# Performance work log

Hardware: AMD Instinct MI355X
Metric: run time of the kernel (lower is better)

## Reference

```python
import jax, jax.numpy as jnp
import numpy as np

B0, PER, T, V, E = 8, 2, 128, 50257, 4
N = B0 * PER


def setup_inputs() -> dict:
    key = jax.random.key(0)
    k1, k2, k3, k4 = jax.random.split(key, 4)
    return {
        "gen_ori_img_preds": jax.random.normal(k1, (B0, T, V), dtype=jnp.float32),
        "gen_cap_preds": jax.random.normal(k2, (N, T, V), dtype=jnp.float32),
        "masked_item_lens": jnp.full((B0,), PER, dtype=jnp.int32),
        "entities_ids": jax.random.randint(k3, (N, E), 0, V, dtype=jnp.int32),
        "prefixes_lens": jax.random.randint(k4, (N,), 1, T, dtype=jnp.int32),  # unused by forward
        "prompt_length": 20,  # unused by forward
    }


def reference(gen_ori_img_preds, gen_cap_preds, masked_item_lens, entities_ids, prefixes_lens, prompt_length):
    # gen_ori_img_preds: [B0, T, V]; gen_cap_preds: [N, T, V]; entities_ids: [N, E]
    B0_, T_, _ = gen_ori_img_preds.shape
    N_ = gen_cap_preds.shape[0]
    # repeat_interleave(arange(B0), masked_item_lens) -> map each expanded row to its source sample
    repeated = jnp.repeat(jnp.arange(B0_), masked_item_lens, total_repeat_length=N_)  # [N]
    # log_softmax gathered at entity columns: log_softmax(x)[..., e] = x[..., e] - logsumexp(x)
    lse_ori = jax.nn.logsumexp(gen_ori_img_preds, axis=-1)  # [B0, T]
    lse_gen = jax.nn.logsumexp(gen_cap_preds, axis=-1)      # [N, T]
    t_idx = jnp.arange(T_)[None, :, None]
    # gather raw logits at entity ids, broadcast over T -> [N, T, E]
    g_ori = gen_ori_img_preds[repeated[:, None, None], t_idx, entities_ids[:, None, :]] \
            - lse_ori[repeated][:, :, None]
    g_gen = jnp.take_along_axis(gen_cap_preds, entities_ids[:, None, :], axis=2) \
            - lse_gen[:, :, None]
    # mean over T per entity, difference, then mean over entities (sum / len(entity_ids_i))
    per_entity = g_ori.mean(axis=1) - g_gen.mean(axis=1)  # [N, E]
    sample_loss = per_entity.mean(axis=-1)                 # [N]
    return (-sample_loss).mean()
```

## Files before the change

### kernel.cpp

```cpp
#include <hip/hip_runtime.h>

#define B0 8
#define T  128
#define V  50257
#define E  4
#define NN 16

__global__ __launch_bounds__(256) void lse_kernel(
    const float* __restrict__ ori, const float* __restrict__ cap,
    float* __restrict__ lse) {
  const int row = blockIdx.x;
  const float* base;
  long long s;
  if (row < B0 * T) {
    base = ori;
    s = (long long)row * V;
  } else {
    base = cap;
    s = (long long)(row - B0 * T) * V;
  }
  const long long end = s + V;
  const long long s_al = (s + 3) & ~3LL;
  const int tid = threadIdx.x;

  float a0 = 0.f, a1 = 0.f, a2 = 0.f, a3 = 0.f;

  const int head = (int)(s_al - s);
  if (tid < head) a0 += __expf(base[s + tid]);

  const long long n4 = (end - s_al) >> 2;
  const float4* b4 = (const float4*)(base + s_al);
  for (long long j = tid; j < n4; j += 256) {
    const float4 v = b4[j];
    a0 += __expf(v.x);
    a1 += __expf(v.y);
    a2 += __expf(v.z);
    a3 += __expf(v.w);
  }

  const long long tstart = s_al + (n4 << 2);
  const int tail = (int)(end - tstart);
  if (tid < tail) a1 += __expf(base[tstart + tid]);

  float acc = (a0 + a1) + (a2 + a3);

  __shared__ float red[256];
  red[tid] = acc;
  __syncthreads();
  for (int w = 128; w > 0; w >>= 1) {
    if (tid < w) red[tid] += red[tid + w];
    __syncthreads();
  }
  if (tid == 0) lse[row] = __logf(red[0]);
}

__global__ __launch_bounds__(256) void finish_kernel(
    const float* __restrict__ ori, const float* __restrict__ cap,
    const int* __restrict__ mlens, const int* __restrict__ eids,
    const float* __restrict__ lse, float* __restrict__ out) {
  __shared__ int rep[NN];
  const int tid = threadIdx.x;
  if (tid == 0) {
    int idx = 0;
    for (int b = 0; b < B0 && idx < NN; ++b) {
      const int c = mlens[b];
      for (int k = 0; k < c && idx < NN; ++k) rep[idx++] = b;
    }
    const int lastv = (idx > 0) ? rep[idx - 1] : 0;
    for (; idx < NN; ++idx) rep[idx] = lastv;
  }
  __syncthreads();

  const float* lse_ori = lse;
  const float* lse_gen = lse + B0 * T;

  float sg = 0.f;
  for (int i = tid; i < NN * E * T; i += 256) {
    const int n = i / (E * T);
    const int r = i - n * (E * T);
    const int e = r / T;
    const int t = r - e * T;
    const int col = eids[n * E + e];
    sg += ori[((long long)rep[n] * T + t) * V + col]
        - cap[((long long)n * T + t) * V + col];
  }

  float sl = 0.f;
  for (int i = tid; i < NN * T; i += 256) {
    const int n = i / T;
    const int t = i - n * T;
    sl += lse_gen[n * T + t] - lse_ori[rep[n] * T + t];
  }

  __shared__ float r1[256];
  __shared__ float r2[256];
  r1[tid] = sg;
  r2[tid] = sl;
  __syncthreads();
  for (int w = 128; w > 0; w >>= 1) {
    if (tid < w) {
      r1[tid] += r1[tid + w];
      r2[tid] += r2[tid + w];
    }
    __syncthreads();
  }
  if (tid == 0) {
    out[0] = -(r1[0] / (float)(NN * E * T) + r2[0] / (float)(NN * T));
  }
}

extern "C" void kernel_launch(void* const* d_in, const int* in_sizes, int n_in,
                              void* d_out, int out_size, void* d_ws, size_t ws_size,
                              hipStream_t stream) {
  const float* ori   = (const float*)d_in[0];
  const float* cap   = (const float*)d_in[1];
  const int*   mlens = (const int*)d_in[2];
  const int*   eids  = (const int*)d_in[3];
  float* out = (float*)d_out;
  float* lse = (float*)d_ws;

  const int rows = B0 * T + NN * T;
  lse_kernel<<<rows, 256, 0, stream>>>(ori, cap, lse);
  finish_kernel<<<1, 256, 0, stream>>>(ori, cap, mlens, eids, lse, out);
}
```

Measured before the change: 695.0 us.

## Fuse LSE and final reduction into one kernel with atomic last-block finish

Merges the per-row logsumexp kernel and the single-block finish kernel into one kernel. Each row block adds its own entity-logit gathers and weighted LSE contribution to a global double accumulator, and the last block to arrive, found through an atomic counter, writes the output. This removes the serial single-block tail kernel and the LSE workspace round trip, at the cost of a memset, per-block atomics and a changed floating-point summation order.

```diff
diff --git a/kernel.cpp b/kernel.cpp
--- a/kernel.cpp
+++ b/kernel.cpp
@@ -5,24 +5,36 @@
 #define V  50257
 #define E  4
 #define NN 16
+#define ROWS_ORI (B0 * T)
+#define ROWS_ALL (B0 * T + NN * T)
 
-__global__ __launch_bounds__(256) void lse_kernel(
+__global__ __launch_bounds__(256) void nde_fused_kernel(
     const float* __restrict__ ori, const float* __restrict__ cap,
-    float* __restrict__ lse) {
+    const int* __restrict__ mlens, const int* __restrict__ eids,
+    double* __restrict__ acc, unsigned int* __restrict__ counter,
+    float* __restrict__ out) {
   const int row = blockIdx.x;
-  const float* base;
-  long long s;
-  if (row < B0 * T) {
-    base = ori;
-    s = (long long)row * V;
-  } else {
-    base = cap;
-    s = (long long)(row - B0 * T) * V;
+  const int tid = threadIdx.x;
+  const bool is_ori = row < ROWS_ORI;
+  const int local_row = is_ori ? row : row - ROWS_ORI;
+  const float* __restrict__ base = is_ori ? ori : cap;
+  const long long s = (long long)local_row * V;
+  const long long end = s + V;
+
+  __shared__ float red[256];
+  __shared__ int rep[NN];
+
+  if (tid == 0) {
+    int idx = 0;
+    for (int b = 0; b < B0 && idx < NN; ++b) {
+      const int c = mlens[b];
+      for (int k = 0; k < c && idx < NN; ++k) rep[idx++] = b;
+    }
+    const int lastv = (idx > 0) ? rep[idx - 1] : 0;
+    for (; idx < NN; ++idx) rep[idx] = lastv;
   }
-  const long long end = s + V;
+
   const long long s_al = (s + 3) & ~3LL;
-  const int tid = threadIdx.x;
-
   float a0 = 0.f, a1 = 0.f, a2 = 0.f, a3 = 0.f;
 
   const int head = (int)(s_al - s);
@@ -42,70 +54,59 @@
   const int tail = (int)(end - tstart);
   if (tid < tail) a1 += __expf(base[tstart + tid]);
 
-  float acc = (a0 + a1) + (a2 + a3);
-
-  __shared__ float red[256];
-  red[tid] = acc;
+  red[tid] = (a0 + a1) + (a2 + a3);
   __syncthreads();
   for (int w = 128; w > 0; w >>= 1) {
     if (tid < w) red[tid] += red[tid + w];
     __syncthreads();
   }
-  if (tid == 0) lse[row] = __logf(red[0]);
-}
 
-__global__ __launch_bounds__(256) void finish_kernel(
-    const float* __restrict__ ori, const float* __restrict__ cap,
-    const int* __restrict__ mlens, const int* __restrict__ eids,
-    const float* __restrict__ lse, float* __restrict__ out) {
-  __shared__ int rep[NN];
-  const int tid = threadIdx.x;
+  const int bn = local_row / T;
+  const float inv_get = 1.0f / (float)(NN * E * T);
+  const float inv_nt  = 1.0f / (float)(NN * T);
+
+  float c = 0.f;
+  if (is_ori) {
+    if (tid < NN * E) {
+      const int n = tid >> 2;
+      if (rep[n] == bn) {
+        const int col = eids[tid];
+        c = base[s + col] * inv_get;
+      }
+    }
+  } else {
+    if (tid < E) {
+      const int col = eids[bn * E + tid];
+      c = -base[s + col] * inv_get;
+    }
+  }
   if (tid == 0) {
-    int idx = 0;
-    for (int b = 0; b < B0 && idx < NN; ++b) {
-      const int c = mlens[b];
-      for (int k = 0; k < c && idx < NN; ++k) rep[idx++] = b;
+    const float lse = __logf(red[0]);
+    if (is_ori) {
+      int w = 0;
+      for (int n = 0; n < NN; ++n) w += (rep[n] == bn);
+      c += -(float)w * lse * inv_nt;
+    } else {
+      c += lse * inv_nt;
     }
-    const int lastv = (idx > 0) ? rep[idx - 1] : 0;
-    for (; idx < NN; ++idx) rep[idx] = lastv;
-  }
-  __syncthreads();
-
-  const float* lse_ori = lse;
-  const float* lse_gen = lse + B0 * T;
-
-  float sg = 0.f;
-  for (int i = tid; i < NN * E * T; i += 256) {
-    const int n = i / (E * T);
-    const int r = i - n * (E * T);
-    const int e = r / T;
-    const int t = r - e * T;
-    const int col = eids[n * E + e];
-    sg += ori[((long long)rep[n] * T + t) * V + col]
-        - cap[((long long)n * T + t) * V + col];
   }
 
-  float sl = 0.f;
-  for (int i = tid; i < NN * T; i += 256) {
-    const int n = i / T;
-    const int t = i - n * T;
-    sl += lse_gen[n * T + t] - lse_ori[rep[n] * T + t];
+  __syncthreads();
+  red[tid] = c;
+  __syncthreads();
+  for (int w = 128; w > 0; w >>= 1) {
+    if (tid < w) red[tid] += red[tid + w];
+    __syncthreads();
   }
 
-  __shared__ float r1[256];
-  __shared__ float r2[256];
-  r1[tid] = sg;
-  r2[tid] = sl;
-  __syncthreads();
-  for (int w = 128; w > 0; w >>= 1) {
-    if (tid < w) {
-      r1[tid] += r1[tid + w];
-      r2[tid] += r2[tid + w];
+  if (tid == 0) {
+    atomicAdd(acc, (double)red[0]);
+    __threadfence();
+    const unsigned int old = atomicAdd(counter, 1u);
+    if (old == (unsigned int)(ROWS_ALL - 1)) {
+      const double total = atomicAdd(acc, 0.0);
+      out[0] = (float)(-total);
     }
-    __syncthreads();
-  }
-  if (tid == 0) {
-    out[0] = -(r1[0] / (float)(NN * E * T) + r2[0] / (float)(NN * T));
   }
 }
 
@@ -117,9 +118,11 @@
   const int*   mlens = (const int*)d_in[2];
   const int*   eids  = (const int*)d_in[3];
   float* out = (float*)d_out;
-  float* lse = (float*)d_ws;
 
-  const int rows = B0 * T + NN * T;
-  lse_kernel<<<rows, 256, 0, stream>>>(ori, cap, lse);
-  finish_kernel<<<1, 256, 0, stream>>>(ori, cap, mlens, eids, lse, out);
+  double* acc = (double*)d_ws;
+  unsigned int* counter = (unsigned int*)((char*)d_ws + 8);
+
+  hipMemsetAsync(d_ws, 0, 16, stream);
+  nde_fused_kernel<<<ROWS_ALL, 256, 0, stream>>>(ori, cap, mlens, eids, acc,
+                                                 counter, out);
 }
```

Result: slower. 779.2 us (+12.1%).
